# Optimization experiments

Hardware: AMD Instinct MI355X
Metric: run time of the kernel (lower is better)

The kernel has to match this reference:

```python
import jax, jax.numpy as jnp
import numpy as np

P = 0.1  # error_prob from init_kwargs


def setup_inputs() -> dict:
    key = jax.random.key(0)
    k1, k2, k3 = jax.random.split(key, 3)
    B, L, V = 4096, 32, 256
    u = jax.random.uniform(k1, (B, L, V), dtype=jnp.float32)
    messages = u / u.sum(-1, keepdims=True)  # per-symbol probability distributions
    entropy = jax.random.uniform(k2, (B, L), dtype=jnp.float32)
    noise = jax.random.uniform(k3, (B, L, V - 1), dtype=jnp.float32)
    return {"messages": messages, "entropy": entropy, "noise": noise}


def reference(messages, entropy, noise):
    # Faithful to SymmetricChannel.gs training branch, vectorized over the
    # message-length loop in Channel.forward.
    B, L, V = messages.shape
    # target mask over the V-1 non-EOS columns of probs[:, 1:]
    mask = noise < jnp.asarray(P, noise.dtype)  # [B, L, V-1], col j of slice
    # Original code computes adjustment[b, j-1] -= probs[b, j-1] for each
    # masked j (note the off-by-one with Python negative wrap: j=0 -> col V-1),
    # then calls scatter_ on a fancy-indexed COPY (a torch no-op). Net effect:
    # probs column (j-1) mod V is zeroed wherever mask[..., j] is True.
    # Masked j in [0, V-2] map to distinct probs columns; column V-2 is never hit.
    zero_col = jnp.zeros(mask.shape[:-1] + (1,), dtype=bool)
    full_mask = jnp.concatenate([mask[..., 1:], zero_col, mask[..., :1]], axis=-1)  # [B,L,V]
    out = jnp.where(full_mask, jnp.zeros((), messages.dtype), messages)

    # entropy += binary_entropy(p) + log2(V - 2)  (constant per symbol)
    p = jnp.asarray(P, entropy.dtype)
    q = 1.0 - p
    min_real = jnp.finfo(entropy.dtype).min
    hb = -(p * jnp.clip(jnp.log2(p), min_real) + q * jnp.clip(jnp.log2(q), min_real))
    const = hb + jnp.log2(jnp.asarray(V - 2, entropy.dtype))
    sym_ent = entropy + const  # [B, L]

    # entropy_dict fields: message, symbol, message_nn, symbol_nn
    return out, sym_ent.sum(-1), sym_ent, entropy.sum(-1), entropy
```

## Files before the change

kernel.cpp:

```cpp
#include <hip/hip_runtime.h>
#include <hip/hip_bf16.h>


__global__ void __launch_bounds__(256) chan_mask_kernel(
    const float4* __restrict__ msg4,
    const float*  __restrict__ noise,
    float4* __restrict__ out4,
    int nvec)
{
    const int stride = gridDim.x * blockDim.x;
    for (int v = blockIdx.x * blockDim.x + threadIdx.x; v < nvec; v += stride) {
        const int row = v >> 6;
        const int k0  = (v & 63) << 2;
        const float* nrow = noise + row * 255;
        float4 m = msg4[v];
        float n0, n1, n2, n3;
        if (k0 != 252) {
            n0 = nrow[k0 + 1];
            n1 = nrow[k0 + 2];
            n2 = nrow[k0 + 3];
            n3 = nrow[k0 + 4];
        } else {
            n0 = nrow[253];
            n1 = nrow[254];
            n2 = 1.0f;
            n3 = nrow[0];
        }
        m.x = (n0 < 0.1f) ? 0.0f : m.x;
        m.y = (n1 < 0.1f) ? 0.0f : m.y;
        m.z = (n2 < 0.1f) ? 0.0f : m.z;
        m.w = (n3 < 0.1f) ? 0.0f : m.w;
        out4[v] = m;
    }
}

__global__ void __launch_bounds__(256) ent_kernel(
    const float* __restrict__ entropy,
    float* __restrict__ o_sym_sum,
    float* __restrict__ o_sym,
    float* __restrict__ o_ent_sum,
    float* __restrict__ o_ent,
    int n)
{
    const float C = (float)8.457680280361447;
    int i = blockIdx.x * blockDim.x + threadIdx.x;
    if (i >= n) return;
    float e = entropy[i];
    o_sym[i] = e + C;
    o_ent[i] = e;
    float es = e;
    #pragma unroll
    for (int m = 1; m < 32; m <<= 1) es += __shfl_xor(es, m);
    if ((threadIdx.x & 31) == 0) {
        int row = i >> 5;
        o_ent_sum[row] = es;
        o_sym_sum[row] = es + 32.0f * C;
    }
}

extern "C" void kernel_launch(void* const* d_in, const int* in_sizes, int n_in,
                              void* d_out, int out_size, void* d_ws, size_t ws_size,
                              hipStream_t stream) {
    const float* messages = (const float*)d_in[0];
    const float* entropy  = (const float*)d_in[1];
    const float* noise    = (const float*)d_in[2];

    float* out = (float*)d_out;
    const int BLV  = 4096 * 32 * 256;
    const int BL   = 4096 * 32;
    const int B    = 4096;

    float* o_out     = out;
    float* o_sym_sum = out + BLV;
    float* o_sym     = o_sym_sum + B;
    float* o_ent_sum = o_sym + BL;
    float* o_ent     = o_ent_sum + B;

    const int nvec = BLV / 4;
    const int blk = 256;
    const int grid1 = 2048;
    chan_mask_kernel<<<grid1, blk, 0, stream>>>(
        (const float4*)messages, noise, (float4*)o_out, nvec);

    const int grid2 = (BL + blk - 1) / blk;
    ent_kernel<<<grid2, blk, 0, stream>>>(
        entropy, o_sym_sum, o_sym, o_ent_sum, o_ent, BL);
}
```

Baseline: 316.5 us.

## Stage noise rows in shared memory with float4 loads, one block per 16 rows

Each block now handles 16 rows. It copies their noise block into LDS with aligned float4 loads, because RPB*255 is divisible by 4, instead of doing four unaligned scalar global loads per thread. Message loads are issued before the staging so they overlap it, and the grid-stride loop is replaced by a fixed grid of BL/16 blocks. The cost is a __syncthreads per block plus LDS reads that may hit bank conflicts because of the 255-float row stride.

```diff
diff --git a/kernel.cpp b/kernel.cpp
--- a/kernel.cpp
+++ b/kernel.cpp
@@ -2,18 +2,39 @@
 #include <hip/hip_bf16.h>
 
 
+#define RPB 16
+
 __global__ void __launch_bounds__(256) chan_mask_kernel(
     const float4* __restrict__ msg4,
-    const float*  __restrict__ noise,
-    float4* __restrict__ out4,
-    int nvec)
+    const float4* __restrict__ noise4,
+    float4* __restrict__ out4)
 {
-    const int stride = gridDim.x * blockDim.x;
-    for (int v = blockIdx.x * blockDim.x + threadIdx.x; v < nvec; v += stride) {
-        const int row = v >> 6;
-        const int k0  = (v & 63) << 2;
-        const float* nrow = noise + row * 255;
-        float4 m = msg4[v];
+    __shared__ float nz[RPB * 255];
+    const int t = threadIdx.x;
+    const int blk = blockIdx.x;
+    const int base = blk * (RPB * 64);
+
+    float4 m0 = msg4[base + t];
+    float4 m1 = msg4[base + t + 256];
+    float4 m2 = msg4[base + t + 512];
+    float4 m3 = msg4[base + t + 768];
+
+    const float4* nsrc = noise4 + blk * (RPB * 255 / 4);
+    #pragma unroll
+    for (int j = 0; j < 4; ++j) {
+        int idx = t + 256 * j;
+        if (idx < RPB * 255 / 4)
+            *reinterpret_cast<float4*>(&nz[4 * idx]) = nsrc[idx];
+    }
+    __syncthreads();
+
+    float4 mm[4] = {m0, m1, m2, m3};
+    #pragma unroll
+    for (int j = 0; j < 4; ++j) {
+        int f = t + 256 * j;
+        int row = f >> 6;
+        int k0 = (f & 63) << 2;
+        const float* nrow = &nz[row * 255];
         float n0, n1, n2, n3;
         if (k0 != 252) {
             n0 = nrow[k0 + 1];
@@ -26,11 +47,12 @@
             n2 = 1.0f;
             n3 = nrow[0];
         }
+        float4 m = mm[j];
         m.x = (n0 < 0.1f) ? 0.0f : m.x;
         m.y = (n1 < 0.1f) ? 0.0f : m.y;
         m.z = (n2 < 0.1f) ? 0.0f : m.z;
         m.w = (n3 < 0.1f) ? 0.0f : m.w;
-        out4[v] = m;
+        out4[base + f] = m;
     }
 }
 
@@ -66,9 +88,9 @@
     const float* noise    = (const float*)d_in[2];
 
     float* out = (float*)d_out;
-    const int BLV  = 4096 * 32 * 256;
-    const int BL   = 4096 * 32;
-    const int B    = 4096;
+    const int BLV = 4096 * 32 * 256;
+    const int BL  = 4096 * 32;
+    const int B   = 4096;
 
     float* o_out     = out;
     float* o_sym_sum = out + BLV;
@@ -76,11 +98,10 @@
     float* o_ent_sum = o_sym + BL;
     float* o_ent     = o_ent_sum + B;
 
-    const int nvec = BLV / 4;
     const int blk = 256;
-    const int grid1 = 2048;
+    const int grid1 = BL / RPB;
     chan_mask_kernel<<<grid1, blk, 0, stream>>>(
-        (const float4*)messages, noise, (float4*)o_out, nvec);
+        (const float4*)messages, (const float4*)noise, (float4*)o_out);
 
     const int grid2 = (BL + blk - 1) / blk;
     ent_kernel<<<grid2, blk, 0, stream>>>(
```

New measurement: 314.7 us. Within noise of the previous version (-0.6%).
